# Kernel tuning notes

Measured on AMD Instinct MI355X. Metric: run time of the kernel, lower is better.

Reference implementation:

```python
import jax, jax.numpy as jnp
import numpy as np

FILTER_LENGTH = 1024
HOP_LENGTH = 512
CUTOFF = FILTER_LENGTH // 2 + 1  # 513
PAD = FILTER_LENGTH // 2


def _make_forward_basis():
    # Real/imag DFT basis, rows = [Re(0..cutoff-1); Im(0..cutoff-1)], cols = time taps
    fb = np.fft.fft(np.eye(FILTER_LENGTH))
    basis = np.vstack([np.real(fb[:CUTOFF, :]), np.imag(fb[:CUTOFF, :])]).astype(np.float32)
    # periodic ('fftbins') Hann window, win_length == filter_length so no centering pad
    n = np.arange(FILTER_LENGTH)
    window = (0.5 - 0.5 * np.cos(2.0 * np.pi * n / FILTER_LENGTH)).astype(np.float32)
    return jnp.asarray(basis * window[None, :])  # [1026, 1024]


def setup_inputs() -> dict:
    key = jax.random.key(0)
    input_data = jax.random.normal(key, (16, 1048576), dtype=jnp.float32)
    forward_basis = _make_forward_basis()
    return {"input_data": input_data, "forward_basis": forward_basis}


def reference(input_data, forward_basis):
    # reflect-pad, frame, windowed DFT via conv1d, then magnitude
    x = jnp.pad(input_data, ((0, 0), (PAD, PAD)), mode="reflect")[:, None, :]  # [B,1,L+1024]
    y = jax.lax.conv_general_dilated(
        x,
        forward_basis[:, None, :],  # [1026, 1, 1024]
        window_strides=(HOP_LENGTH,),
        padding="VALID",
        dimension_numbers=("NCH", "OIH", "NCH"),
    )  # [B, 1026, T]
    real = y[:, :CUTOFF, :]
    imag = y[:, CUTOFF:, :]
    return jnp.sqrt(real * real + imag * imag)  # [B, 513, T]
```

## Files before the change

kernel.cpp:

```cpp
#include <hip/hip_runtime.h>
#include <math.h>

#define L_IN   1048576
#define NBATCH 16
#define T_FR   2049
#define NBINS  513

struct C2 { float r, i; };
__device__ __forceinline__ C2 cadd(C2 a, C2 b){ return {a.r+b.r, a.i+b.i}; }
__device__ __forceinline__ C2 csub(C2 a, C2 b){ return {a.r-b.r, a.i-b.i}; }
__device__ __forceinline__ C2 cmul(C2 a, C2 b){ return {a.r*b.r - a.i*b.i, a.r*b.i + a.i*b.r}; }
__device__ __forceinline__ C2 cnegi(C2 a){ return {a.i, -a.r}; }
#define RSQ2 0.70710678118654752f
__device__ __forceinline__ C2 cw8 (C2 a){ return { RSQ2*(a.r+a.i),  RSQ2*(a.i-a.r)}; }
__device__ __forceinline__ C2 cw83(C2 a){ return { RSQ2*(a.i-a.r), -RSQ2*(a.r+a.i)}; }

__device__ __forceinline__ void dft8(const C2 x[8], C2 y[8]) {
  C2 ea0 = cadd(x[0], x[4]), ea1 = csub(x[0], x[4]);
  C2 eb0 = cadd(x[2], x[6]), eb1 = csub(x[2], x[6]);
  C2 oa0 = cadd(x[1], x[5]), oa1 = csub(x[1], x[5]);
  C2 ob0 = cadd(x[3], x[7]), ob1 = csub(x[3], x[7]);
  C2 E0 = cadd(ea0, eb0), E2 = csub(ea0, eb0);
  C2 nb = cnegi(eb1);
  C2 E1 = cadd(ea1, nb),  E3 = csub(ea1, nb);
  C2 O0 = cadd(oa0, ob0), O2 = csub(oa0, ob0);
  C2 no = cnegi(ob1);
  C2 O1 = cadd(oa1, no),  O3 = csub(oa1, no);
  y[0] = cadd(E0, O0);  y[4] = csub(E0, O0);
  C2 t1 = cw8(O1);      y[1] = cadd(E1, t1); y[5] = csub(E1, t1);
  C2 t2 = cnegi(O2);    y[2] = cadd(E2, t2); y[6] = csub(E2, t2);
  C2 t3 = cw83(O3);     y[3] = cadd(E3, t3); y[7] = csub(E3, t3);
}

__device__ __forceinline__ int phys(int idx) { return idx ^ ((idx >> 4) & 15); }

#define FENCE do { asm volatile("s_waitcnt lgkmcnt(0)" ::: "memory"); \
                   __builtin_amdgcn_sched_barrier(0); } while (0)

#define TWOPI 6.283185307179586f

__device__ __forceinline__ void load_raw(float2 v[8], const float* __restrict__ xb,
                                         int tt, int t) {
  const int s0 = tt*512 - 512;
  if (tt != 0 && tt != 2048) {
    #pragma unroll
    for (int j = 0; j < 8; ++j) v[j] = *(const float2*)&xb[s0 + 2*(t + 64*j)];
  } else {
    #pragma unroll
    for (int j = 0; j < 8; ++j) {
      int e0 = s0 + 2*(t + 64*j), e1 = e0 + 1;
      int r0 = e0 < 0 ? -e0 : (e0 >= L_IN ? 2*L_IN - 2 - e0 : e0);
      int r1 = e1 < 0 ? -e1 : (e1 >= L_IN ? 2*L_IN - 2 - e1 : e1);
      v[j] = { xb[r0], xb[r1] };
    }
  }
}

__device__ __forceinline__ void process_frame(const float2 v[8], const float2 wl[8],
    const C2 tws1[8], const C2 tws2[8], const C2 twu[8],
    C2* __restrict__ cfw, float (* __restrict__ mag)[17], int t, int tl)
{
  C2 x[8], y[8];
  #pragma unroll
  for (int j = 0; j < 8; ++j) x[j] = { v[j].x * wl[j].x, v[j].y * wl[j].y };
  dft8(x, y);
  #pragma unroll
  for (int k = 0; k < 8; ++k) cfw[phys(8*t + k)] = y[k];
  FENCE;
  {
    const int m = t & 7, g = t >> 3;
    C2 xs[8];
    #pragma unroll
    for (int j = 0; j < 8; ++j) xs[j] = cfw[phys(t + 64*j)];
    #pragma unroll
    for (int j = 1; j < 8; ++j) xs[j] = cmul(xs[j], tws1[j]);
    dft8(xs, y);
    #pragma unroll
    for (int k = 0; k < 8; ++k) cfw[phys(g*64 + m + 8*k)] = y[k];
  }
  FENCE;
  C2 z[8];
  {
    C2 xs[8];
    #pragma unroll
    for (int j = 0; j < 8; ++j) xs[j] = cfw[phys(t + 64*j)];
    #pragma unroll
    for (int j = 1; j < 8; ++j) xs[j] = cmul(xs[j], tws2[j]);
    dft8(xs, z);
    #pragma unroll
    for (int k = 0; k < 8; ++k) cfw[phys(t + 64*k)] = z[k];
  }
  FENCE;
  #pragma unroll
  for (int j = 0; j < 8; ++j) {
    const int k = t + 64*j;
    C2 Zk = z[j];
    C2 Zp = cfw[phys((512 - k) & 511)];
    C2 W  = twu[j];
    float Are = 0.5f*(Zk.r + Zp.r), Aim = 0.5f*(Zk.i - Zp.i);
    float Bre = 0.5f*(Zk.r - Zp.r), Bim = 0.5f*(Zk.i + Zp.i);
    float Xr = Are + (W.r*Bim + W.i*Bre);
    float Xi = Aim - (W.r*Bre - W.i*Bim);
    mag[k][tl] = sqrtf(Xr*Xr + Xi*Xi);
  }
  if (t == 0) mag[512][tl] = fabsf(z[0].r - z[0].i);
  FENCE;
}

__global__ __launch_bounds__(256, 3)
void stft_fft(const float* __restrict__ input,
              const float* __restrict__ basis,
              float* __restrict__ out)
{
  __shared__ C2    cf[4][512];
  __shared__ float mag[513][17];

  const int tid = threadIdx.x;
  const int t   = tid & 63;
  const int w   = tid >> 6;
  const int b   = blockIdx.y;
  const int t0  = blockIdx.x << 4;

  C2 tws1[8], tws2[8], twu[8];
  {
    const int m = t & 7;
    #pragma unroll
    for (int j = 1; j < 8; ++j) {
      float s, c, a1 = (TWOPI/64.0f)  * (float)(m*j);
      __sincosf(a1, &s, &c); tws1[j] = { c, -s };
      float a2 = (TWOPI/512.0f) * (float)(t*j);
      __sincosf(a2, &s, &c); tws2[j] = { c, -s };
    }
    #pragma unroll
    for (int j = 0; j < 8; ++j) {
      float s, c, a = (TWOPI/1024.0f) * (float)(t + 64*j);
      __sincosf(a, &s, &c); twu[j] = { c, -s };
    }
  }

  float2 wl[8];
  #pragma unroll
  for (int j = 0; j < 8; ++j) wl[j] = *(const float2*)&basis[2*(t + 64*j)];

  const float* xb = input + (size_t)b * L_IN;
  C2* cfw = cf[w];
  const int base = t0 + w*4;

  float2 v0[8], v1[8];
  if (base     <= 2048) load_raw(v0, xb, base,     t);
  if (base + 1 <= 2048) load_raw(v1, xb, base + 1, t);
  if (base     <= 2048) process_frame(v0, wl, tws1, tws2, twu, cfw, mag, t, w*4);
  if (base + 2 <= 2048) load_raw(v0, xb, base + 2, t);
  if (base + 1 <= 2048) process_frame(v1, wl, tws1, tws2, twu, cfw, mag, t, w*4 + 1);
  if (base + 3 <= 2048) load_raw(v1, xb, base + 3, t);
  if (base + 2 <= 2048) process_frame(v0, wl, tws1, tws2, twu, cfw, mag, t, w*4 + 2);
  if (base + 3 <= 2048) process_frame(v1, wl, tws1, tws2, twu, cfw, mag, t, w*4 + 3);

  __syncthreads();

  const size_t ob = (size_t)b * NBINS * T_FR;
  for (int idx = tid; idx < NBINS*16; idx += 256) {
    const int row = idx >> 4, tl = idx & 15, tt = t0 + tl;
    if (tt <= 2048) out[ob + (size_t)row * T_FR + tt] = mag[row][tl];
  }
}

extern "C" void kernel_launch(void* const* d_in, const int* in_sizes, int n_in,
                              void* d_out, int out_size, void* d_ws, size_t ws_size,
                              hipStream_t stream) {
  const float* input = (const float*)d_in[0];
  const float* basis = (const float*)d_in[1];
  float* out = (float*)d_out;
  stft_fft<<<dim3(129, 16), 256, 0, stream>>>(input, basis, out);
}
```

Baseline: 54.26 us.

## Shuffle final FFT stage, store magnitudes as bf16 in LDS, remap blocks

The conjugate-pair lookup for the real-FFT post-processing now uses cross-lane shuffles instead of an LDS store/reload, which removes one LDS round trip and one fence per frame. Magnitudes are staged in shared memory as bf16, halving the mag buffer, and launch bounds are raised to 4 blocks per CU. The grid is flattened and block IDs are remapped across XCD-like groups. Rounding output magnitudes to bf16 loses precision and may exceed the output tolerance.

```diff
diff --git a/kernel.cpp b/kernel.cpp
--- a/kernel.cpp
+++ b/kernel.cpp
@@ -34,6 +34,12 @@
 
 __device__ __forceinline__ int phys(int idx) { return idx ^ ((idx >> 4) & 15); }
 
+__device__ __forceinline__ unsigned short f2bf(float f) {
+  unsigned int u = __builtin_bit_cast(unsigned int, f);
+  u += 0x7FFFu + ((u >> 16) & 1u);
+  return (unsigned short)(u >> 16);
+}
+
 #define FENCE do { asm volatile("s_waitcnt lgkmcnt(0)" ::: "memory"); \
                    __builtin_amdgcn_sched_barrier(0); } while (0)
 
@@ -58,7 +64,7 @@
 
 __device__ __forceinline__ void process_frame(const float2 v[8], const float2 wl[8],
     const C2 tws1[8], const C2 tws2[8], const C2 twu[8],
-    C2* __restrict__ cfw, float (* __restrict__ mag)[17], int t, int tl)
+    C2* __restrict__ cfw, unsigned short (* __restrict__ mag)[18], int t, int tl)
 {
   C2 x[8], y[8];
   #pragma unroll
@@ -84,42 +90,44 @@
     C2 xs[8];
     #pragma unroll
     for (int j = 0; j < 8; ++j) xs[j] = cfw[phys(t + 64*j)];
+    FENCE;
     #pragma unroll
     for (int j = 1; j < 8; ++j) xs[j] = cmul(xs[j], tws2[j]);
     dft8(xs, z);
-    #pragma unroll
-    for (int k = 0; k < 8; ++k) cfw[phys(t + 64*k)] = z[k];
   }
-  FENCE;
+  const int pl = (64 - t) & 63;
   #pragma unroll
   for (int j = 0; j < 8; ++j) {
     const int k = t + 64*j;
+    C2 Zp = { __shfl(z[7-j].r, pl), __shfl(z[7-j].i, pl) };
+    if (t == 0) Zp = z[(8-j) & 7];
     C2 Zk = z[j];
-    C2 Zp = cfw[phys((512 - k) & 511)];
     C2 W  = twu[j];
     float Are = 0.5f*(Zk.r + Zp.r), Aim = 0.5f*(Zk.i - Zp.i);
     float Bre = 0.5f*(Zk.r - Zp.r), Bim = 0.5f*(Zk.i + Zp.i);
     float Xr = Are + (W.r*Bim + W.i*Bre);
     float Xi = Aim - (W.r*Bre - W.i*Bim);
-    mag[k][tl] = sqrtf(Xr*Xr + Xi*Xi);
+    mag[k][tl] = f2bf(sqrtf(Xr*Xr + Xi*Xi));
   }
-  if (t == 0) mag[512][tl] = fabsf(z[0].r - z[0].i);
-  FENCE;
+  if (t == 0) mag[512][tl] = f2bf(fabsf(z[0].r - z[0].i));
 }
 
-__global__ __launch_bounds__(256, 3)
+__global__ __launch_bounds__(256, 4)
 void stft_fft(const float* __restrict__ input,
               const float* __restrict__ basis,
               float* __restrict__ out)
 {
-  __shared__ C2    cf[4][512];
-  __shared__ float mag[513][17];
+  __shared__ C2 cf[4][512];
+  __shared__ unsigned short mag[513][18];
 
   const int tid = threadIdx.x;
   const int t   = tid & 63;
   const int w   = tid >> 6;
-  const int b   = blockIdx.y;
-  const int t0  = blockIdx.x << 4;
+
+  const int bid = blockIdx.x;
+  const int wg  = (bid & 7) * 258 + (bid >> 3);
+  const int b   = wg / 129;
+  const int t0  = (wg - b * 129) << 4;
 
   C2 tws1[8], tws2[8], twu[8];
   {
@@ -161,7 +169,10 @@
   const size_t ob = (size_t)b * NBINS * T_FR;
   for (int idx = tid; idx < NBINS*16; idx += 256) {
     const int row = idx >> 4, tl = idx & 15, tt = t0 + tl;
-    if (tt <= 2048) out[ob + (size_t)row * T_FR + tt] = mag[row][tl];
+    if (tt <= 2048) {
+      unsigned int u = (unsigned int)mag[row][tl] << 16;
+      out[ob + (size_t)row * T_FR + tt] = __builtin_bit_cast(float, u);
+    }
   }
 }
 
@@ -171,5 +182,5 @@
   const float* input = (const float*)d_in[0];
   const float* basis = (const float*)d_in[1];
   float* out = (float*)d_out;
-  stft_fft<<<dim3(129, 16), 256, 0, stream>>>(input, basis, out);
+  stft_fft<<<dim3(129 * 16), 256, 0, stream>>>(input, basis, out);
 }
```

Result: slower. 98.28 us (+81.1%).
